# Kernel tuning notes

Hardware: AMD Instinct MI355X
Metric: run time of the kernel (lower is better)

Reference implementation:

```python
import jax, jax.numpy as jnp
import numpy as np

N = 100000   # nodes
E = 1600000  # edges
D = 128      # input_dim
H = 128      # hidden_dim
O = 64       # output_dim


def setup_inputs() -> dict:
    key = jax.random.key(0)
    ks = jax.random.split(key, 8)
    x = jax.random.normal(ks[0], (N, D), dtype=jnp.float32)
    edge_index = jax.random.randint(ks[1], (2, E), 0, N, dtype=jnp.int32)
    # Glorot-ish init for weights, zeros for biases (matches GCNConv/Linear defaults in spirit)
    W1 = jax.random.normal(ks[2], (D, H), dtype=jnp.float32) / np.sqrt(D)
    b1 = jnp.zeros((H,), dtype=jnp.float32)
    W2 = jax.random.normal(ks[3], (H, H), dtype=jnp.float32) / np.sqrt(H)
    b2 = jnp.zeros((H,), dtype=jnp.float32)
    Wf = jax.random.normal(ks[4], (H, O), dtype=jnp.float32) / np.sqrt(H)
    bf = jnp.zeros((O,), dtype=jnp.float32)
    return {"x": x, "W1": W1, "b1": b1, "W2": W2, "b2": b2,
            "Wf": Wf, "bf": bf, "edge_index": edge_index}


def gcn_conv(x, W, b, src, dst):
    """GCNConv: out = D^{-1/2} (A + I) D^{-1/2} (x W) + b, edges given as (src->dst)."""
    n = x.shape[0]
    h = x @ W  # [N, H]
    loop = jnp.arange(n, dtype=src.dtype)
    s = jnp.concatenate([src, loop])  # add self-loops
    d = jnp.concatenate([dst, loop])
    deg = jax.ops.segment_sum(jnp.ones_like(s, dtype=h.dtype), d, num_segments=n)
    dinv = jnp.where(deg > 0, jax.lax.rsqrt(deg), 0.0)
    coef = dinv[s] * dinv[d]                              # [E+N]
    msg = h[s] * coef[:, None]                            # gather + scale
    out = jax.ops.segment_sum(msg, d, num_segments=n)     # scatter-add aggregate
    return out + b


def reference(x, W1, b1, W2, b2, Wf, bf, edge_index):
    src, dst = edge_index[0], edge_index[1]
    h = jax.nn.relu(gcn_conv(x, W1, b1, src, dst))
    # dropout is identity in eval mode
    h = jax.nn.relu(gcn_conv(h, W2, b2, src, dst))
    return h @ Wf + bf
```

## Files before the change

kernel.cpp:

```cpp
#include <hip/hip_runtime.h>

#define FD 128
#define SCAN_B 256
#define SCAN_T 256

typedef __attribute__((ext_vector_type(8))) short bf16x8;
typedef __attribute__((ext_vector_type(4))) float f32x4;


__global__ void k_deg(const int* __restrict__ dst, int* __restrict__ deg,
                      int* __restrict__ rank, int E) {
  int e = blockIdx.x * blockDim.x + threadIdx.x;
  if (e < E) rank[e] = atomicAdd(&deg[dst[e]], 1);
}


__global__ __launch_bounds__(SCAN_T) void k_part(const int* __restrict__ deg,
                                                 float* __restrict__ dinv,
                                                 int* __restrict__ part, int n) {
  const int b = blockIdx.x;
  const int chunk = (n + SCAN_B - 1) / SCAN_B;
  const int lo = b * chunk;
  const int hi = min(lo + chunk, n);
  int sum = 0;
  for (int i = lo + threadIdx.x; i < hi; i += SCAN_T) {
    int d = deg[i];
    sum += d;
    dinv[i] = rsqrtf((float)(d + 1));
  }
  __shared__ int red[SCAN_T / 64];
  for (int off = 32; off > 0; off >>= 1) sum += __shfl_down(sum, off, 64);
  if ((threadIdx.x & 63) == 0) red[threadIdx.x >> 6] = sum;
  __syncthreads();
  if (threadIdx.x == 0) {
    int s = 0;
#pragma unroll
    for (int w = 0; w < SCAN_T / 64; ++w) s += red[w];
    part[b] = s;
  }
}

__global__ __launch_bounds__(SCAN_B) void k_scanpart(int* __restrict__ part,
                                                     int* __restrict__ row_ptr, int n) {
  __shared__ int s[SCAN_B];
  const int t = threadIdx.x;
  int v = part[t];
  s[t] = v;
  __syncthreads();
  for (int off = 1; off < SCAN_B; off <<= 1) {
    int u = (t >= off) ? s[t - off] : 0;
    __syncthreads();
    s[t] += u;
    __syncthreads();
  }
  part[t] = s[t] - v;
  if (t == SCAN_B - 1) row_ptr[n] = s[t];
}

__global__ __launch_bounds__(SCAN_T) void k_rowptr(const int* __restrict__ deg,
                                                   const int* __restrict__ part,
                                                   int* __restrict__ row_ptr, int n) {
  const int b = blockIdx.x;
  const int chunk = (n + SCAN_B - 1) / SCAN_B;
  const int lo = b * chunk;
  const int hi = min(lo + chunk, n);
  const int sub = (chunk + SCAN_T - 1) / SCAN_T;
  const int t = threadIdx.x;
  const int slo = min(lo + t * sub, hi);
  const int shi = min(slo + sub, hi);
  int sum = 0;
  for (int i = slo; i < shi; ++i) sum += deg[i];
  __shared__ int s[SCAN_T];
  s[t] = sum;
  __syncthreads();
  for (int off = 1; off < SCAN_T; off <<= 1) {
    int u = (t >= off) ? s[t - off] : 0;
    __syncthreads();
    s[t] += u;
    __syncthreads();
  }
  int run = part[b] + s[t] - sum;
  for (int i = slo; i < shi; ++i) {
    row_ptr[i] = run;
    run += deg[i];
  }
}


__global__ void k_fill(const int* __restrict__ src, const int* __restrict__ dst,
                       const int* __restrict__ rank, const int* __restrict__ row_ptr,
                       int* __restrict__ csr_src, int E) {
  int e = blockIdx.x * blockDim.x + threadIdx.x;
  if (e < E) {
    csr_src[row_ptr[dst[e]] + rank[e]] = src[e];
  }
}


__device__ __forceinline__ void split_bf16(float x, short& hi, short& lo) {
  unsigned u = __float_as_uint(x);
  unsigned short h = (unsigned short)((u + 0x7fffu + ((u >> 16) & 1u)) >> 16);
  float hf = __uint_as_float((unsigned)h << 16);
  unsigned ul = __float_as_uint(x - hf);
  hi = (short)h;
  lo = (short)((ul + 0x7fffu + ((ul >> 16) & 1u)) >> 16);
}

__global__ __launch_bounds__(256) void k_gemm(const float* __restrict__ A, int lda,
                                              const float* __restrict__ W, int ldw,
                                              const float* __restrict__ bias,
                                              float* __restrict__ out, int ldo, int nrows) {
  __shared__ short xhi[64][136], xlo[64][136];
  __shared__ short whi[64][136], wlo[64][136];
  const int t  = threadIdx.x;
  const int r0 = blockIdx.x * 64;
  const int c0 = blockIdx.y * 64;

  {
    const int row  = t >> 2;
    const int kb   = (t & 3) * 32;
    const int grow = r0 + row;
    const float* ap = &A[(size_t)grow * lda + kb];
#pragma unroll
    for (int j = 0; j < 8; ++j) {
      float4 v = make_float4(0.f, 0.f, 0.f, 0.f);
      if (grow < nrows) v = *reinterpret_cast<const float4*>(ap + 4 * j);
      short4 h4, l4;
      split_bf16(v.x, h4.x, l4.x);
      split_bf16(v.y, h4.y, l4.y);
      split_bf16(v.z, h4.z, l4.z);
      split_bf16(v.w, h4.w, l4.w);
      *reinterpret_cast<short4*>(&xhi[row][kb + 4 * j]) = h4;
      *reinterpret_cast<short4*>(&xlo[row][kb + 4 * j]) = l4;
    }
  }
  {
    const int k  = t >> 1;
    const int cb = (t & 1) * 32;
    const float* wp = &W[(size_t)k * ldw + c0 + cb];
#pragma unroll
    for (int j = 0; j < 8; ++j) {
      float4 v = *reinterpret_cast<const float4*>(wp + 4 * j);
      short h, l;
      split_bf16(v.x, h, l); whi[cb + 4 * j + 0][k] = h; wlo[cb + 4 * j + 0][k] = l;
      split_bf16(v.y, h, l); whi[cb + 4 * j + 1][k] = h; wlo[cb + 4 * j + 1][k] = l;
      split_bf16(v.z, h, l); whi[cb + 4 * j + 2][k] = h; wlo[cb + 4 * j + 2][k] = l;
      split_bf16(v.w, h, l); whi[cb + 4 * j + 3][k] = h; wlo[cb + 4 * j + 3][k] = l;
    }
  }
  __syncthreads();

  const int w  = t >> 6;
  const int l  = t & 63;
  const int lr = l & 15;
  const int lk = l >> 4;

  f32x4 acc[4] = {};
#pragma unroll
  for (int kc = 0; kc < 4; ++kc) {
    const int kb = kc * 32 + lk * 8;
    const bf16x8 ah = *reinterpret_cast<const bf16x8*>(&xhi[w * 16 + lr][kb]);
    const bf16x8 al = *reinterpret_cast<const bf16x8*>(&xlo[w * 16 + lr][kb]);
#pragma unroll
    for (int ct = 0; ct < 4; ++ct) {
      const bf16x8 bh = *reinterpret_cast<const bf16x8*>(&whi[ct * 16 + lr][kb]);
      const bf16x8 bl = *reinterpret_cast<const bf16x8*>(&wlo[ct * 16 + lr][kb]);
      acc[ct] = __builtin_amdgcn_mfma_f32_16x16x32_bf16(ah, bh, acc[ct], 0, 0, 0);
      acc[ct] = __builtin_amdgcn_mfma_f32_16x16x32_bf16(ah, bl, acc[ct], 0, 0, 0);
      acc[ct] = __builtin_amdgcn_mfma_f32_16x16x32_bf16(al, bh, acc[ct], 0, 0, 0);
    }
  }

#pragma unroll
  for (int ct = 0; ct < 4; ++ct) {
    const int col = c0 + ct * 16 + lr;
    const float b = bias ? bias[col] : 0.f;
#pragma unroll
    for (int r = 0; r < 4; ++r) {
      const int row = r0 + w * 16 + lk * 4 + r;
      if (row < nrows) out[(size_t)row * ldo + col] = acc[ct][r] + b;
    }
  }
}


__global__ __launch_bounds__(256) void k_agg(const float* __restrict__ h,
                                             const int* __restrict__ row_ptr,
                                             const int* __restrict__ csr_src,
                                             const float* __restrict__ dinv,
                                             const float* __restrict__ bias,
                                             float* __restrict__ out, int n) {
  const int node = blockIdx.x * 4 + (threadIdx.x >> 6);
  if (node >= n) return;
  const int lane = threadIdx.x & 63;
  const int sub  = lane >> 5;
  const int c4   = (lane & 31) << 2;
  const float di = dinv[node];

  float4 acc = make_float4(0.f, 0.f, 0.f, 0.f);
  const int e0 = row_ptr[node], e1 = row_ptr[node + 1];
  int e = e0;
  for (; e + 8 <= e1; e += 8) {
    const int ia = csr_src[e     + sub];
    const int ib = csr_src[e + 2 + sub];
    const int ic = csr_src[e + 4 + sub];
    const int id = csr_src[e + 6 + sub];
    const float4 va = *reinterpret_cast<const float4*>(&h[(size_t)ia * FD + c4]);
    const float4 vb = *reinterpret_cast<const float4*>(&h[(size_t)ib * FD + c4]);
    const float4 vc = *reinterpret_cast<const float4*>(&h[(size_t)ic * FD + c4]);
    const float4 vd = *reinterpret_cast<const float4*>(&h[(size_t)id * FD + c4]);
    const float ca = dinv[ia] * di;
    const float cb = dinv[ib] * di;
    const float cc = dinv[ic] * di;
    const float cd = dinv[id] * di;
    acc.x += va.x * ca + vb.x * cb + vc.x * cc + vd.x * cd;
    acc.y += va.y * ca + vb.y * cb + vc.y * cc + vd.y * cd;
    acc.z += va.z * ca + vb.z * cb + vc.z * cc + vd.z * cd;
    acc.w += va.w * ca + vb.w * cb + vc.w * cc + vd.w * cd;
  }
  for (; e + 2 <= e1; e += 2) {
    const int i0 = csr_src[e + sub];
    const float4 v = *reinterpret_cast<const float4*>(&h[(size_t)i0 * FD + c4]);
    const float c = dinv[i0] * di;
    acc.x += v.x * c; acc.y += v.y * c; acc.z += v.z * c; acc.w += v.w * c;
  }
  if (e < e1 && sub == 0) {
    const int i0 = csr_src[e];
    const float4 v = *reinterpret_cast<const float4*>(&h[(size_t)i0 * FD + c4]);
    const float c = dinv[i0] * di;
    acc.x += v.x * c; acc.y += v.y * c; acc.z += v.z * c; acc.w += v.w * c;
  }

  acc.x += __shfl_xor(acc.x, 32);
  acc.y += __shfl_xor(acc.y, 32);
  acc.z += __shfl_xor(acc.z, 32);
  acc.w += __shfl_xor(acc.w, 32);

  const float4 hs = *reinterpret_cast<const float4*>(&h[(size_t)node * FD + c4]);
  const float4 b4 = *reinterpret_cast<const float4*>(&bias[c4]);
  float4 o;
  o.x = fmaxf(acc.x + hs.x * di * di + b4.x, 0.f);
  o.y = fmaxf(acc.y + hs.y * di * di + b4.y, 0.f);
  o.z = fmaxf(acc.z + hs.z * di * di + b4.z, 0.f);
  o.w = fmaxf(acc.w + hs.w * di * di + b4.w, 0.f);
  if (sub == 0)
    *reinterpret_cast<float4*>(&out[(size_t)node * FD + c4]) = o;
}


extern "C" void kernel_launch(void* const* d_in, const int* in_sizes, int n_in,
                              void* d_out, int out_size, void* d_ws, size_t ws_size,
                              hipStream_t stream) {
  const float* x  = (const float*)d_in[0];
  const float* W1 = (const float*)d_in[1];
  const float* b1 = (const float*)d_in[2];
  const float* W2 = (const float*)d_in[3];
  const float* b2 = (const float*)d_in[4];
  const float* Wf = (const float*)d_in[5];
  const float* bf = (const float*)d_in[6];
  const int*   ei = (const int*)d_in[7];

  const int N = in_sizes[0] / FD;
  const int E = in_sizes[7] / 2;
  const int O = in_sizes[6];
  const int* src = ei;
  const int* dst = ei + E;

  char* ws = (char*)d_ws;
  size_t off = 0;
  auto alloc = [&](size_t bytes) -> void* {
    void* p = ws + off;
    off += (bytes + 255) & ~(size_t)255;
    return p;
  };
  float* A       = (float*)alloc((size_t)N * FD * 4);
  float* B       = (float*)alloc((size_t)N * FD * 4);
  int*   deg     = (int*)  alloc((size_t)N * 4);
  float* dinv    = (float*)alloc((size_t)N * 4);
  int*   row_ptr = (int*)  alloc((size_t)(N + 1) * 4);
  int*   rank    = (int*)  alloc((size_t)E * 4);
  int*   csr_src = (int*)  alloc((size_t)E * 4);
  int*   part    = (int*)  alloc((size_t)SCAN_B * 4);

  hipMemsetAsync(deg, 0, (size_t)N * 4, stream);
  k_deg     <<<(E + 255) / 256, 256, 0, stream>>>(dst, deg, rank, E);
  k_part    <<<SCAN_B, SCAN_T, 0, stream>>>(deg, dinv, part, N);
  k_scanpart<<<1, SCAN_B, 0, stream>>>(part, row_ptr, N);
  k_rowptr  <<<SCAN_B, SCAN_T, 0, stream>>>(deg, part, row_ptr, N);
  k_fill    <<<(E + 255) / 256, 256, 0, stream>>>(src, dst, rank, row_ptr, csr_src, E);

  const int gx = (N + 63) / 64;
  k_gemm<<<dim3(gx, 2), 256, 0, stream>>>(x, FD, W1, FD, nullptr, A, FD, N);
  k_agg <<<(N + 3) / 4, 256, 0, stream>>>(A, row_ptr, csr_src, dinv, b1, B, N);
  k_gemm<<<dim3(gx, 2), 256, 0, stream>>>(B, FD, W2, FD, nullptr, A, FD, N);
  k_agg <<<(N + 3) / 4, 256, 0, stream>>>(A, row_ptr, csr_src, dinv, b2, B, N);
  k_gemm<<<dim3(gx, 1), 256, 0, stream>>>(B, FD, Wf, O, bf, (float*)d_out, O, N);
}
```

Baseline: 602.3 us.

## Fold partial-sum scan into rowptr kernel and co-launch CSR fill with first GEMM

Drops the single-block scan kernel: every k_rowptr block now redundantly scans the 256 partial sums in shared memory. The CSR fill and the first GEMM are merged into one heterogeneous launch, with leading blocks doing the edge scatter and the rest doing GEMM tiles, so the two independent stages can overlap and two launches go away. The cost is that fill blocks reserve the GEMM's large static shared-memory footprint, which may reduce their occupancy, and a little redundant scan work per block.

```diff
diff --git a/kernel.cpp b/kernel.cpp
--- a/kernel.cpp
+++ b/kernel.cpp
@@ -40,37 +40,33 @@
   }
 }
 
-__global__ __launch_bounds__(SCAN_B) void k_scanpart(int* __restrict__ part,
-                                                     int* __restrict__ row_ptr, int n) {
-  __shared__ int s[SCAN_B];
-  const int t = threadIdx.x;
-  int v = part[t];
-  s[t] = v;
-  __syncthreads();
-  for (int off = 1; off < SCAN_B; off <<= 1) {
-    int u = (t >= off) ? s[t - off] : 0;
-    __syncthreads();
-    s[t] += u;
-    __syncthreads();
-  }
-  part[t] = s[t] - v;
-  if (t == SCAN_B - 1) row_ptr[n] = s[t];
-}
 
 __global__ __launch_bounds__(SCAN_T) void k_rowptr(const int* __restrict__ deg,
                                                    const int* __restrict__ part,
                                                    int* __restrict__ row_ptr, int n) {
+  __shared__ int ps[SCAN_B];
+  __shared__ int s[SCAN_T];
+  const int t = threadIdx.x;
   const int b = blockIdx.x;
+  ps[t] = part[t];
+  __syncthreads();
+  for (int off = 1; off < SCAN_B; off <<= 1) {
+    int u = (t >= off) ? ps[t - off] : 0;
+    __syncthreads();
+    ps[t] += u;
+    __syncthreads();
+  }
+  const int excl = (b == 0) ? 0 : ps[b - 1];
+  if (b == 0 && t == 0) row_ptr[n] = ps[SCAN_B - 1];
+
   const int chunk = (n + SCAN_B - 1) / SCAN_B;
   const int lo = b * chunk;
   const int hi = min(lo + chunk, n);
   const int sub = (chunk + SCAN_T - 1) / SCAN_T;
-  const int t = threadIdx.x;
   const int slo = min(lo + t * sub, hi);
   const int shi = min(slo + sub, hi);
   int sum = 0;
   for (int i = slo; i < shi; ++i) sum += deg[i];
-  __shared__ int s[SCAN_T];
   s[t] = sum;
   __syncthreads();
   for (int off = 1; off < SCAN_T; off <<= 1) {
@@ -79,20 +75,10 @@
     s[t] += u;
     __syncthreads();
   }
-  int run = part[b] + s[t] - sum;
+  int run = excl + s[t] - sum;
   for (int i = slo; i < shi; ++i) {
     row_ptr[i] = run;
     run += deg[i];
-  }
-}
-
-
-__global__ void k_fill(const int* __restrict__ src, const int* __restrict__ dst,
-                       const int* __restrict__ rank, const int* __restrict__ row_ptr,
-                       int* __restrict__ csr_src, int E) {
-  int e = blockIdx.x * blockDim.x + threadIdx.x;
-  if (e < E) {
-    csr_src[row_ptr[dst[e]] + rank[e]] = src[e];
   }
 }
 
@@ -106,16 +92,12 @@
   lo = (short)((ul + 0x7fffu + ((ul >> 16) & 1u)) >> 16);
 }
 
-__global__ __launch_bounds__(256) void k_gemm(const float* __restrict__ A, int lda,
-                                              const float* __restrict__ W, int ldw,
-                                              const float* __restrict__ bias,
-                                              float* __restrict__ out, int ldo, int nrows) {
-  __shared__ short xhi[64][136], xlo[64][136];
-  __shared__ short whi[64][136], wlo[64][136];
-  const int t  = threadIdx.x;
-  const int r0 = blockIdx.x * 64;
-  const int c0 = blockIdx.y * 64;
-
+
+__device__ __forceinline__ void gemm_body(
+    short (*xhi)[136], short (*xlo)[136], short (*whi)[136], short (*wlo)[136],
+    int t, int r0, int c0,
+    const float* __restrict__ A, int lda, const float* __restrict__ W, int ldw,
+    const float* __restrict__ bias, float* __restrict__ out, int ldo, int nrows) {
   {
     const int row  = t >> 2;
     const int kb   = (t & 3) * 32;
@@ -181,6 +163,37 @@
       if (row < nrows) out[(size_t)row * ldo + col] = acc[ct][r] + b;
     }
   }
+}
+
+
+__global__ __launch_bounds__(256) void k_fill_gemm(
+    const int* __restrict__ src, const int* __restrict__ dst,
+    const int* __restrict__ rank, const int* __restrict__ row_ptr,
+    int* __restrict__ csr_src, int E, int nfb,
+    const float* __restrict__ A, int lda, const float* __restrict__ W, int ldw,
+    float* __restrict__ out, int ldo, int nrows, int gx) {
+  __shared__ short xhi[64][136], xlo[64][136];
+  __shared__ short whi[64][136], wlo[64][136];
+  const int t = threadIdx.x;
+  if ((int)blockIdx.x < nfb) {
+    const int e = blockIdx.x * 256 + t;
+    if (e < E) csr_src[row_ptr[dst[e]] + rank[e]] = src[e];
+    return;
+  }
+  const int gid = (int)blockIdx.x - nfb;
+  gemm_body(xhi, xlo, whi, wlo, t, (gid % gx) * 64, (gid / gx) * 64,
+            A, lda, W, ldw, nullptr, out, ldo, nrows);
+}
+
+
+__global__ __launch_bounds__(256) void k_gemm(const float* __restrict__ A, int lda,
+                                              const float* __restrict__ W, int ldw,
+                                              const float* __restrict__ bias,
+                                              float* __restrict__ out, int ldo, int nrows) {
+  __shared__ short xhi[64][136], xlo[64][136];
+  __shared__ short whi[64][136], wlo[64][136];
+  gemm_body(xhi, xlo, whi, wlo, threadIdx.x, blockIdx.x * 64, blockIdx.y * 64,
+            A, lda, W, ldw, bias, out, ldo, nrows);
 }
 
 
@@ -282,15 +295,16 @@
   int*   csr_src = (int*)  alloc((size_t)E * 4);
   int*   part    = (int*)  alloc((size_t)SCAN_B * 4);
 
+  const int gx  = (N + 63) / 64;
+  const int nfb = (E + 255) / 256;
+
   hipMemsetAsync(deg, 0, (size_t)N * 4, stream);
-  k_deg     <<<(E + 255) / 256, 256, 0, stream>>>(dst, deg, rank, E);
-  k_part    <<<SCAN_B, SCAN_T, 0, stream>>>(deg, dinv, part, N);
-  k_scanpart<<<1, SCAN_B, 0, stream>>>(part, row_ptr, N);
-  k_rowptr  <<<SCAN_B, SCAN_T, 0, stream>>>(deg, part, row_ptr, N);
-  k_fill    <<<(E + 255) / 256, 256, 0, stream>>>(src, dst, rank, row_ptr, csr_src, E);
-
-  const int gx = (N + 63) / 64;
-  k_gemm<<<dim3(gx, 2), 256, 0, stream>>>(x, FD, W1, FD, nullptr, A, FD, N);
+  k_deg   <<<(E + 255) / 256, 256, 0, stream>>>(dst, deg, rank, E);
+  k_part  <<<SCAN_B, SCAN_T, 0, stream>>>(deg, dinv, part, N);
+  k_rowptr<<<SCAN_B, SCAN_T, 0, stream>>>(deg, part, row_ptr, N);
+
+  k_fill_gemm<<<nfb + 2 * gx, 256, 0, stream>>>(src, dst, rank, row_ptr, csr_src, E, nfb,
+                                                x, FD, W1, FD, A, FD, N, gx);
   k_agg <<<(N + 3) / 4, 256, 0, stream>>>(A, row_ptr, csr_src, dinv, b1, B, N);
   k_gemm<<<dim3(gx, 2), 256, 0, stream>>>(B, FD, W2, FD, nullptr, A, FD, N);
   k_agg <<<(N + 3) / 4, 256, 0, stream>>>(A, row_ptr, csr_src, dinv, b2, B, N);
```

After: 573.2 us. -4.8%, faster.
